# Performance work log

Measured on AMD Instinct MI355X. Metric: run time of the kernel, lower is better.

The kernel has to match this reference:

```python
import jax, jax.numpy as jnp
import numpy as np

TOP_K = 512  # int(node_num * K) = int(2048 * 0.25)
NEG = -1.0e12
SLOPE = 0.01  # nn.LeakyReLU default negative_slope


def setup_inputs() -> dict:
    key = jax.random.key(0)
    k1, k2, k3, k4 = jax.random.split(key, 4)
    B, N, in_c, out_c, gs = 8, 2048, 128, 128, 128
    x = jax.random.normal(k1, (B, N, in_c), dtype=jnp.float32)
    W = jax.random.normal(k2, (in_c, out_c), dtype=jnp.float32) * (1.0 / np.sqrt(in_c))
    a = jax.random.normal(k3, (2 * out_c, 1), dtype=jnp.float32) * (1.0 / np.sqrt(2 * out_c))
    GL = jax.random.normal(k4, (N, gs), dtype=jnp.float32) * (1.0 / np.sqrt(gs))
    return {"x": x, "W": W, "a": a, "GL": GL}


def reference(x, W, a, GL):
    B, N, _ = x.shape
    out_c = W.shape[1]
    # learned adjacency: softmax(relu(GL GL^T)) + I  -> [N, N]
    adj = jax.nn.softmax(jax.nn.relu(GL @ GL.T), axis=-1) + jnp.eye(N, dtype=GL.dtype)
    h = x @ W  # [B, N, out_c]
    # e[b,i,j] = LeakyReLU( [h_i ; h_j] . a ) = LeakyReLU( h_i.a1 + h_j.a2 )
    # (avoids materializing the [B, N*N, 2*out_c] concat of the original)
    a1, a2 = a[:out_c, 0], a[out_c:, 0]
    e = jax.nn.leaky_relu((h @ a1)[:, :, None] + (h @ a2)[:, None, :], SLOPE)  # [B,N,N]
    att = jnp.where(adj[None] > 0, e, NEG)
    # top-k along dim=1 (rows, per column j): transpose so that axis is last
    att_t = jnp.swapaxes(att, 1, 2)  # [B, Nj, Ni]
    _, idx = jax.lax.top_k(att_t, TOP_K)  # idx: [B, Nj, TOP_K]
    b_ix = jnp.arange(B)[:, None, None]
    j_ix = jnp.arange(N)[None, :, None]
    mask_t = jnp.zeros_like(att_t).at[b_ix, j_ix, idx].set(1.0)
    mask = jnp.swapaxes(mask_t, 1, 2)  # [B, Ni, Nj]
    att = jax.nn.softmax(att * mask, axis=2)
    h_prime = jax.nn.relu(att @ h)  # [B, N, out_c]
    return jnp.swapaxes(h_prime, -2, -1)  # [B, out_c, N]
```

## Files before the change

### kernel.cpp

```cpp
#include <hip/hip_runtime.h>
#include <math.h>


#define B_ 8
#define N_ 2048
#define C_ 128
#define TOPK_ 512
#define NCH_ 32
#define CL_ 64
#define NP1_ 2052
#define RANKB_ 256

#define H_OFF    ((size_t)0)
#define P_OFF    (H_OFF + (size_t)B_*N_*C_)
#define Q_OFF    (P_OFF + (size_t)B_*N_)
#define LOK_OFF  (Q_OFF + (size_t)B_*N_)
#define US_OFF   (LOK_OFF + (size_t)B_*N_)
#define VS_OFF   (US_OFF + (size_t)B_*N_)
#define SRT_OFF  (VS_OFF + (size_t)B_*N_)
#define SUS_OFF  (SRT_OFF + (size_t)B_*N_)
#define PVS_OFF  (SUS_OFF + (size_t)B_*NP1_)
#define SUL_OFF  (PVS_OFF + (size_t)B_*NP1_)
#define PVL_OFF  (SUL_OFF + (size_t)B_*N_*128)
#define TOTU_OFF (PVL_OFF + (size_t)B_*N_*128)
#define TOTV_OFF (TOTU_OFF + (size_t)B_*NCH_*128)
#define MPART_OFF (TOTV_OFF + (size_t)B_*NCH_*128)

__global__ __launch_bounds__(256) void k_pq(const float* __restrict__ x,
                                            const float* __restrict__ W,
                                            const float* __restrict__ a,
                                            float* __restrict__ p,
                                            float* __restrict__ q) {
  __shared__ float al[256];
  __shared__ float wa1[128], wa2[128];
  const int t = threadIdx.x;
  const int r0 = blockIdx.x * 64;
  al[t] = a[t];
  __syncthreads();
  if (t < 128) {
    const float* Wr = W + (size_t)t * 128;
    float s1 = 0.f, s2 = 0.f;
#pragma unroll
    for (int j = 0; j < 128; j += 4) {
      float4 wv = *(const float4*)(Wr + j);
      s1 = fmaf(wv.x, al[j + 0], s1);
      s1 = fmaf(wv.y, al[j + 1], s1);
      s1 = fmaf(wv.z, al[j + 2], s1);
      s1 = fmaf(wv.w, al[j + 3], s1);
      s2 = fmaf(wv.x, al[128 + j + 0], s2);
      s2 = fmaf(wv.y, al[128 + j + 1], s2);
      s2 = fmaf(wv.z, al[128 + j + 2], s2);
      s2 = fmaf(wv.w, al[128 + j + 3], s2);
    }
    wa1[t] = s1; wa2[t] = s2;
  }
  __syncthreads();
  const int row = t >> 2, part = t & 3;
  const float* xr = x + (size_t)(r0 + row) * 128 + part * 32;
  const float* w1 = wa1 + part * 32;
  const float* w2 = wa2 + part * 32;
  float sp = 0.f, sq = 0.f;
#pragma unroll
  for (int i = 0; i < 8; ++i) {
    float4 xv = *(const float4*)(xr + 4 * i);
    float4 w1v = *(const float4*)(w1 + 4 * i);
    float4 w2v = *(const float4*)(w2 + 4 * i);
    sp = fmaf(xv.x, w1v.x, sp); sp = fmaf(xv.y, w1v.y, sp);
    sp = fmaf(xv.z, w1v.z, sp); sp = fmaf(xv.w, w1v.w, sp);
    sq = fmaf(xv.x, w2v.x, sq); sq = fmaf(xv.y, w2v.y, sq);
    sq = fmaf(xv.z, w2v.z, sq); sq = fmaf(xv.w, w2v.w, sq);
  }
  sp += __shfl_xor(sp, 1, 64); sp += __shfl_xor(sp, 2, 64);
  sq += __shfl_xor(sq, 1, 64); sq += __shfl_xor(sq, 2, 64);
  if (part == 0) { p[r0 + row] = sp; q[r0 + row] = sq; }
}

__global__ __launch_bounds__(512, 4) void k_fuse(
    const float* __restrict__ x, const float* __restrict__ W,
    float* __restrict__ h, float* __restrict__ mpart,
    const float* __restrict__ q, const float* __restrict__ p,
    float* __restrict__ u_s, float* __restrict__ v_s,
    int* __restrict__ srt, int* __restrict__ lok) {
  union __align__(16) SMem {
    struct { float Wl[64 * 128]; float xl[64 * 68]; } g;
    struct { float ql[N_]; float pl[N_]; } r;
  };
  __shared__ SMem sm;
  const int blk = blockIdx.x, t = threadIdx.x;

  if (blk < RANKB_) {
    const int b = blk >> 5, tile = blk & 31;
    const int i0 = tile * 64;
    ((float4*)sm.r.ql)[t] = ((const float4*)(q + (size_t)b * N_))[t];
    ((float4*)sm.r.pl)[t] = ((const float4*)(p + (size_t)b * N_))[t];
    __syncthreads();
    const int row = t >> 3, s = t & 7;
    const int i = i0 + row;
    const float qi = sm.r.ql[i], pi = sm.r.pl[i];
    const float negpi = -pi;
    int qr = 0, lo = 0, pr = 0;
    for (int g = s; g < 512; g += 8) {
      float4 qj = ((const float4*)sm.r.ql)[g];
      float4 pj = ((const float4*)sm.r.pl)[g];
      const int j0 = 4 * g;
      qr += (qj.x < qi || (qj.x == qi && (j0 + 0) < i)) ? 1 : 0;
      qr += (qj.y < qi || (qj.y == qi && (j0 + 1) < i)) ? 1 : 0;
      qr += (qj.z < qi || (qj.z == qi && (j0 + 2) < i)) ? 1 : 0;
      qr += (qj.w < qi || (qj.w == qi && (j0 + 3) < i)) ? 1 : 0;
      lo += (qj.x < negpi) ? 1 : 0;
      lo += (qj.y < negpi) ? 1 : 0;
      lo += (qj.z < negpi) ? 1 : 0;
      lo += (qj.w < negpi) ? 1 : 0;
      pr += (pj.x > pi || (pj.x == pi && (j0 + 0) < i)) ? 1 : 0;
      pr += (pj.y > pi || (pj.y == pi && (j0 + 1) < i)) ? 1 : 0;
      pr += (pj.z > pi || (pj.z == pi && (j0 + 2) < i)) ? 1 : 0;
      pr += (pj.w > pi || (pj.w == pi && (j0 + 3) < i)) ? 1 : 0;
    }
    qr += __shfl_xor(qr, 1, 64); qr += __shfl_xor(qr, 2, 64); qr += __shfl_xor(qr, 4, 64);
    lo += __shfl_xor(lo, 1, 64); lo += __shfl_xor(lo, 2, 64); lo += __shfl_xor(lo, 4, 64);
    pr += __shfl_xor(pr, 1, 64); pr += __shfl_xor(pr, 2, 64); pr += __shfl_xor(pr, 4, 64);
    if (s == 0) {
      u_s[(size_t)b * N_ + qr] = __expf(qi);
      v_s[(size_t)b * N_ + qr] = __expf(0.01f * qi);
      srt[(size_t)b * N_ + qr] = i;
      lok[(size_t)b * N_ + i] = lo | ((pr < TOPK_) ? 0x10000 : 0);
    }
    return;
  }

  float* Wl = sm.g.Wl;
  float* xl = sm.g.xl;
  const int g = blk - RANKB_;
  const int r0 = g * 64;
  const int cg = t & 15, rp = (t >> 4) & 15;
  const bool act = t < 256;
  float acc[4][8];
#pragma unroll
  for (int r = 0; r < 4; ++r)
#pragma unroll
    for (int j = 0; j < 8; ++j) acc[r][j] = 0.f;

  for (int kc = 0; kc < 2; ++kc) {
    __syncthreads();
    const float4* W4 = (const float4*)(W + (size_t)kc * 64 * 128);
    float4* Wl4 = (float4*)Wl;
#pragma unroll
    for (int i = 0; i < 4; ++i) Wl4[t + 512 * i] = W4[t + 512 * i];
#pragma unroll
    for (int i = 0; i < 2; ++i) {
      int idx = t + 512 * i;
      int row = idx >> 4, c4i = idx & 15;
      float4 v = *(const float4*)(x + (size_t)(r0 + row) * 128 + kc * 64 + c4i * 4);
      ((float4*)xl)[row * 17 + c4i] = v;
    }
    __syncthreads();
    if (act) {
      for (int k = 0; k < 64; ++k) {
        const float4* Wr = (const float4*)(Wl + k * 128);
        float4 w0 = Wr[cg];
        float4 w1 = Wr[cg + 16];
#pragma unroll
        for (int r = 0; r < 4; ++r) {
          float xv = xl[(4 * rp + r) * 68 + k];
          acc[r][0] = fmaf(xv, w0.x, acc[r][0]);
          acc[r][1] = fmaf(xv, w0.y, acc[r][1]);
          acc[r][2] = fmaf(xv, w0.z, acc[r][2]);
          acc[r][3] = fmaf(xv, w0.w, acc[r][3]);
          acc[r][4] = fmaf(xv, w1.x, acc[r][4]);
          acc[r][5] = fmaf(xv, w1.y, acc[r][5]);
          acc[r][6] = fmaf(xv, w1.z, acc[r][6]);
          acc[r][7] = fmaf(xv, w1.w, acc[r][7]);
        }
      }
    }
  }
  const int c0 = 4 * cg, c1 = 4 * cg + 64;
  size_t hb = (size_t)r0 * 128;
  __syncthreads();
  float* scratch = xl;
  if (act) {
#pragma unroll
    for (int r = 0; r < 4; ++r) {
      int row = 4 * rp + r;
      *(float4*)(h + hb + (size_t)row * 128 + c0) =
          make_float4(acc[r][0], acc[r][1], acc[r][2], acc[r][3]);
      *(float4*)(h + hb + (size_t)row * 128 + c1) =
          make_float4(acc[r][4], acc[r][5], acc[r][6], acc[r][7]);
    }
#pragma unroll
    for (int j = 0; j < 4; ++j) {
      scratch[rp * 128 + c0 + j] = acc[0][j] + acc[1][j] + acc[2][j] + acc[3][j];
      scratch[rp * 128 + c1 + j] = acc[0][4 + j] + acc[1][4 + j] + acc[2][4 + j] + acc[3][4 + j];
    }
  }
  __syncthreads();
  if (t < 128) {
    float s = 0.f;
#pragma unroll
    for (int rr = 0; rr < 16; ++rr) s += scratch[rr * 128 + t];
    mpart[(size_t)g * 128 + t] = s;
  }
}

__global__ __launch_bounds__(256) void k_scan(const float* __restrict__ h,
                                              const float* __restrict__ u_s,
                                              const float* __restrict__ v_s,
                                              const int* __restrict__ srt,
                                              float* __restrict__ SUl,
                                              float* __restrict__ PVl,
                                              float* __restrict__ totU,
                                              float* __restrict__ totV,
                                              float* __restrict__ SUS,
                                              float* __restrict__ PVS) {
  __shared__ float hl[CL_][128];
  __shared__ float ul[CL_], vl[CL_];
  __shared__ int sl[CL_];
  __shared__ float2 sa[256], sb[256];
  const int t = threadIdx.x;
  if (blockIdx.x >= 256) {
    const int b = blockIdx.x - 256;
    float4 ua = ((const float4*)(u_s + (size_t)b * N_))[2 * t];
    float4 ub = ((const float4*)(u_s + (size_t)b * N_))[2 * t + 1];
    float4 wa = ((const float4*)(v_s + (size_t)b * N_))[2 * t];
    float4 wb = ((const float4*)(v_s + (size_t)b * N_))[2 * t + 1];
    float su = ua.x + ua.y + ua.z + ua.w + ub.x + ub.y + ub.z + ub.w;
    float sw = wa.x + wa.y + wa.z + wa.w + wb.x + wb.y + wb.z + wb.w;
    sa[t] = make_float2(su, sw);
    __syncthreads();
    float2* cur = sa; float2* nxt = sb;
    for (int off = 1; off < 256; off <<= 1) {
      float2 vv = cur[t];
      if (t >= off) { float2 o = cur[t - off]; vv.x += o.x; vv.y += o.y; }
      nxt[t] = vv;
      __syncthreads();
      float2* tmp = cur; cur = nxt; nxt = tmp;
    }
    float2 incl = cur[t];
    float2 tot = cur[255];
    float exclU = incl.x - su, exclW = incl.y - sw;
    float s0 = tot.x - exclU;
    float s1 = s0 - ua.x, s2 = s1 - ua.y, s3 = s2 - ua.z;
    float s4 = s3 - ua.w, s5 = s4 - ub.x, s6 = s5 - ub.y, s7 = s6 - ub.z;
    float p0 = exclW;
    float p1 = p0 + wa.x, p2 = p1 + wa.y, p3 = p2 + wa.z;
    float p4 = p3 + wa.w, p5 = p4 + wb.x, p6 = p5 + wb.y, p7 = p6 + wb.z;
    float* Sb = SUS + (size_t)b * NP1_ + 8 * t;
    float* Pb = PVS + (size_t)b * NP1_ + 8 * t;
    *(float4*)(Sb) = make_float4(s0, s1, s2, s3);
    *(float4*)(Sb + 4) = make_float4(s4, s5, s6, s7);
    *(float4*)(Pb) = make_float4(p0, p1, p2, p3);
    *(float4*)(Pb + 4) = make_float4(p4, p5, p6, p7);
    if (t == 255) {
      SUS[(size_t)b * NP1_ + N_] = 0.f;
      PVS[(size_t)b * NP1_ + N_] = tot.y;
    }
    return;
  }
  const int b = blockIdx.x >> 5, ch = blockIdx.x & 31;
  const int base = b * N_ + ch * CL_;
  if (t < CL_) { ul[t] = u_s[base + t]; vl[t] = v_s[base + t]; sl[t] = srt[base + t]; }
  __syncthreads();
  {
    const int c4 = t & 31, rr = t >> 5;
#pragma unroll
    for (int i = 0; i < 8; ++i) {
      int tt = rr + 8 * i;
      float4 v = *(const float4*)(h + ((size_t)b * N_ + sl[tt]) * 128 + 4 * c4);
      *(float4*)(&hl[tt][4 * c4]) = v;
    }
  }
  __syncthreads();
  if (t < 128) {
    const int c = t;
    float run = 0.f;
    for (int tt = CL_ - 1; tt >= 0; --tt) {
      run = fmaf(ul[tt], hl[tt][c], run);
      SUl[((size_t)(base + tt)) * 128 + c] = run;
    }
    totU[(size_t)(b * NCH_ + ch) * 128 + c] = run;
  } else {
    const int c = t - 128;
    float run2 = 0.f;
    for (int tt = 0; tt < CL_; ++tt) {
      PVl[((size_t)(base + tt)) * 128 + c] = run2;
      run2 = fmaf(vl[tt], hl[tt][c], run2);
    }
    totV[(size_t)(b * NCH_ + ch) * 128 + c] = run2;
  }
}

__global__ __launch_bounds__(256) void k_out(const float* __restrict__ p,
                                             const int* __restrict__ lok,
                                             const float* __restrict__ SUS,
                                             const float* __restrict__ PVS,
                                             const float* __restrict__ SUl,
                                             const float* __restrict__ PVl,
                                             const float* __restrict__ totU,
                                             const float* __restrict__ totV,
                                             const float* __restrict__ mpart,
                                             float* __restrict__ out) {
  __shared__ float res[64 * 129];
  __shared__ float CSUs[(NCH_ + 1) * 128];
  __shared__ float CPVs[(NCH_ + 1) * 128];
  __shared__ float mr[128];
  __shared__ float A_s[64], B_s[64], invD[64];
  __shared__ int lo_s[64], keep_s[64];
  const int b = blockIdx.x >> 5, tile = blockIdx.x & 31;
  const int t = threadIdx.x;
  const int i0 = tile * 64;
  if (t < 128) {
    float ms = 0.f;
#pragma unroll
    for (int j = 0; j < 32; ++j) ms += mpart[(size_t)(b * 32 + j) * 128 + t];
    mr[t] = fmaxf(ms * (1.0f / (float)N_), 0.f);
    float s = 0.f;
    CSUs[NCH_ * 128 + t] = 0.f;
    for (int cc = NCH_ - 1; cc >= 0; --cc) {
      s += totU[(size_t)(b * NCH_ + cc) * 128 + t];
      CSUs[cc * 128 + t] = s;
    }
  } else {
    const int c2 = t - 128;
    float s2 = 0.f;
    for (int cc = 0; cc < NCH_; ++cc) {
      CPVs[cc * 128 + c2] = s2;
      s2 += totV[(size_t)(b * NCH_ + cc) * 128 + c2];
    }
    CPVs[NCH_ * 128 + c2] = s2;
  }
  __syncthreads();
  if (t < 64) {
    float pv = p[b * N_ + i0 + t];
    int lk = lok[(size_t)b * N_ + i0 + t];
    keep_s[t] = (lk >> 16) & 1;
    int lo = lk & 0xFFFF;
    lo_s[t] = lo;
    float A = __expf(pv), Bv = __expf(0.01f * pv);
    A_s[t] = A; B_s[t] = Bv;
    float sus = SUS[(size_t)b * NP1_ + lo];
    float pvs = PVS[(size_t)b * NP1_ + lo];
    invD[t] = 1.0f / fmaf(A, sus, Bv * pvs);
  }
  __syncthreads();
  const int half = t >> 7, c = t & 127;
#pragma unroll 4
  for (int ii2 = 0; ii2 < 64; ii2 += 2) {
    int ii = ii2 + half;
    float outv;
    if (keep_s[ii]) {
      int lo = lo_s[ii];
      float A = A_s[ii], Bv = B_s[ii];
      float suc, pvc;
      if (lo < N_) {
        int chn = lo >> 6;
        size_t ro = ((size_t)(b * N_ + lo)) * 128;
        suc = SUl[ro + c] + CSUs[(chn + 1) * 128 + c];
        pvc = PVl[ro + c] + CPVs[chn * 128 + c];
      } else {
        suc = 0.f;
        pvc = CPVs[NCH_ * 128 + c];
      }
      outv = fmaxf(fmaf(A, suc, Bv * pvc) * invD[ii], 0.f);
    } else {
      outv = mr[c];
    }
    res[ii * 129 + c] = outv;
  }
  __syncthreads();
#pragma unroll
  for (int pass = 0; pass < 8; ++pass) {
    int cc = (t >> 4) + pass * 16;
    int ii4 = (t & 15) * 4;
    float4 v;
    v.x = res[(ii4 + 0) * 129 + cc];
    v.y = res[(ii4 + 1) * 129 + cc];
    v.z = res[(ii4 + 2) * 129 + cc];
    v.w = res[(ii4 + 3) * 129 + cc];
    *(float4*)(out + ((size_t)(b * C_ + cc)) * N_ + i0 + ii4) = v;
  }
}

extern "C" void kernel_launch(void* const* d_in, const int* in_sizes, int n_in,
                              void* d_out, int out_size, void* d_ws, size_t ws_size,
                              hipStream_t stream) {
  (void)in_sizes; (void)n_in; (void)out_size; (void)ws_size;
  const float* x = (const float*)d_in[0];
  const float* W = (const float*)d_in[1];
  const float* a = (const float*)d_in[2];
  float* out = (float*)d_out;
  float* ws = (float*)d_ws;

  float* h    = ws + H_OFF;
  float* p    = ws + P_OFF;
  float* q    = ws + Q_OFF;
  int*   lok  = (int*)(ws + LOK_OFF);
  float* u_s  = ws + US_OFF;
  float* v_s  = ws + VS_OFF;
  int*   srt  = (int*)(ws + SRT_OFF);
  float* SUS  = ws + SUS_OFF;
  float* PVS  = ws + PVS_OFF;
  float* SUl  = ws + SUL_OFF;
  float* PVl  = ws + PVL_OFF;
  float* totU = ws + TOTU_OFF;
  float* totV = ws + TOTV_OFF;
  float* mpart = ws + MPART_OFF;

  k_pq<<<dim3((B_ * N_) / 64), dim3(256), 0, stream>>>(x, W, a, p, q);
  k_fuse<<<dim3(RANKB_ + (B_ * N_) / 64), dim3(512), 0, stream>>>(
      x, W, h, mpart, q, p, u_s, v_s, srt, lok);
  k_scan<<<dim3(256 + B_), dim3(256), 0, stream>>>(h, u_s, v_s, srt, SUl, PVl, totU, totV, SUS, PVS);
  k_out<<<dim3(B_ * 32), dim3(256), 0, stream>>>(p, lok, SUS, PVS, SUl, PVl, totU, totV, mpart, out);
}
```

Baseline: 104.3 us.

## Merge four kernels into one cooperative persistent kernel with grid syncs

Replaces the four separate launches (pq, gemm+rank, scan, output) with a single cooperative kernel of 256 blocks × 512 threads. Grid-wide syncs separate the phases, and a per-phase launch path is kept as a fallback. The pq computation now runs inside the gemm blocks instead of as its own kernel. This removes launch overhead and the gaps between kernels, but the rank work that previously overlapped with the gemm blocks is now serialized behind a grid barrier, and 256-thread phases leave half of each block idle.

```diff
diff --git a/kernel.cpp b/kernel.cpp
--- a/kernel.cpp
+++ b/kernel.cpp
@@ -1,5 +1,8 @@
 #include <hip/hip_runtime.h>
+#include <hip/hip_cooperative_groups.h>
 #include <math.h>
+
+namespace cg = cooperative_groups;
 
 
 #define B_ 8
@@ -9,7 +12,7 @@
 #define NCH_ 32
 #define CL_ 64
 #define NP1_ 2052
-#define RANKB_ 256
+#define NBLK_ 256
 
 #define H_OFF    ((size_t)0)
 #define P_OFF    (H_OFF + (size_t)B_*N_*C_)
@@ -26,83 +29,157 @@
 #define TOTV_OFF (TOTU_OFF + (size_t)B_*NCH_*128)
 #define MPART_OFF (TOTV_OFF + (size_t)B_*NCH_*128)
 
-__global__ __launch_bounds__(256) void k_pq(const float* __restrict__ x,
-                                            const float* __restrict__ W,
-                                            const float* __restrict__ a,
-                                            float* __restrict__ p,
-                                            float* __restrict__ q) {
-  __shared__ float al[256];
-  __shared__ float wa1[128], wa2[128];
-  const int t = threadIdx.x;
-  const int r0 = blockIdx.x * 64;
-  al[t] = a[t];
-  __syncthreads();
-  if (t < 128) {
-    const float* Wr = W + (size_t)t * 128;
-    float s1 = 0.f, s2 = 0.f;
-#pragma unroll
-    for (int j = 0; j < 128; j += 4) {
-      float4 wv = *(const float4*)(Wr + j);
-      s1 = fmaf(wv.x, al[j + 0], s1);
-      s1 = fmaf(wv.y, al[j + 1], s1);
-      s1 = fmaf(wv.z, al[j + 2], s1);
-      s1 = fmaf(wv.w, al[j + 3], s1);
-      s2 = fmaf(wv.x, al[128 + j + 0], s2);
-      s2 = fmaf(wv.y, al[128 + j + 1], s2);
-      s2 = fmaf(wv.z, al[128 + j + 2], s2);
-      s2 = fmaf(wv.w, al[128 + j + 3], s2);
-    }
-    wa1[t] = s1; wa2[t] = s2;
+union SMem {
+  struct { float Wl[64 * 128]; float xl[64 * 68];
+           float al[256]; float wa1[128]; float wa2[128]; } g;
+  struct { float ql[N_]; float pl[N_]; } r;
+  struct { float hl[CL_][128]; float ul[CL_]; float vl[CL_]; int sl[CL_];
+           float2 sa[256]; float2 sb[256]; } s;
+  struct { float CSU[(NCH_ + 1) * 128]; float CPV[(NCH_ + 1) * 128];
+           float mr[128]; float A[64]; float Bv[64]; float invD[64];
+           int lo[64]; int keep[64]; float res[64 * 129]; } o;
+};
+
+__global__ __launch_bounds__(512, 4) void k_all(
+    const float* __restrict__ x, const float* __restrict__ W,
+    const float* __restrict__ a, float* __restrict__ out,
+    float* __restrict__ h, float* __restrict__ p, float* __restrict__ q,
+    int* __restrict__ lok, float* __restrict__ u_s, float* __restrict__ v_s,
+    int* __restrict__ srt, float* __restrict__ SUS, float* __restrict__ PVS,
+    float* __restrict__ SUl, float* __restrict__ PVl,
+    float* __restrict__ totU, float* __restrict__ totV,
+    float* __restrict__ mpart, int phase) {
+  __shared__ SMem sm;
+  cg::grid_group grid = cg::this_grid();
+  const int blk = blockIdx.x, t = threadIdx.x;
+  const bool all = (phase < 0);
+
+  if (all || phase == 0) {
+    const int r0 = blk * 64;
+    if (t < 256) sm.g.al[t] = a[t];
+    __syncthreads();
+    if (t < 128) {
+      const float* Wr = W + (size_t)t * 128;
+      float s1 = 0.f, s2 = 0.f;
+#pragma unroll
+      for (int j = 0; j < 128; j += 4) {
+        float4 wv = *(const float4*)(Wr + j);
+        s1 = fmaf(wv.x, sm.g.al[j + 0], s1);
+        s1 = fmaf(wv.y, sm.g.al[j + 1], s1);
+        s1 = fmaf(wv.z, sm.g.al[j + 2], s1);
+        s1 = fmaf(wv.w, sm.g.al[j + 3], s1);
+        s2 = fmaf(wv.x, sm.g.al[128 + j + 0], s2);
+        s2 = fmaf(wv.y, sm.g.al[128 + j + 1], s2);
+        s2 = fmaf(wv.z, sm.g.al[128 + j + 2], s2);
+        s2 = fmaf(wv.w, sm.g.al[128 + j + 3], s2);
+      }
+      sm.g.wa1[t] = s1; sm.g.wa2[t] = s2;
+    }
+    __syncthreads();
+    {
+      const int row = t >> 3, part = t & 7;
+      const float* xr = x + (size_t)(r0 + row) * 128 + part * 16;
+      const float* w1 = sm.g.wa1 + part * 16;
+      const float* w2 = sm.g.wa2 + part * 16;
+      float sp = 0.f, sq = 0.f;
+#pragma unroll
+      for (int i = 0; i < 4; ++i) {
+        float4 xv = *(const float4*)(xr + 4 * i);
+        float4 w1v = *(const float4*)(w1 + 4 * i);
+        float4 w2v = *(const float4*)(w2 + 4 * i);
+        sp = fmaf(xv.x, w1v.x, sp); sp = fmaf(xv.y, w1v.y, sp);
+        sp = fmaf(xv.z, w1v.z, sp); sp = fmaf(xv.w, w1v.w, sp);
+        sq = fmaf(xv.x, w2v.x, sq); sq = fmaf(xv.y, w2v.y, sq);
+        sq = fmaf(xv.z, w2v.z, sq); sq = fmaf(xv.w, w2v.w, sq);
+      }
+      sp += __shfl_xor(sp, 1, 64); sp += __shfl_xor(sp, 2, 64); sp += __shfl_xor(sp, 4, 64);
+      sq += __shfl_xor(sq, 1, 64); sq += __shfl_xor(sq, 2, 64); sq += __shfl_xor(sq, 4, 64);
+      if (part == 0) { p[r0 + row] = sp; q[r0 + row] = sq; }
+    }
+    const int cg2 = t & 15, rp = (t >> 4) & 15;
+    const bool act = t < 256;
+    float acc[4][8];
+#pragma unroll
+    for (int r = 0; r < 4; ++r)
+#pragma unroll
+      for (int j = 0; j < 8; ++j) acc[r][j] = 0.f;
+    for (int kc = 0; kc < 2; ++kc) {
+      __syncthreads();
+      const float4* W4 = (const float4*)(W + (size_t)kc * 64 * 128);
+      float4* Wl4 = (float4*)sm.g.Wl;
+#pragma unroll
+      for (int i = 0; i < 4; ++i) Wl4[t + 512 * i] = W4[t + 512 * i];
+#pragma unroll
+      for (int i = 0; i < 2; ++i) {
+        int idx = t + 512 * i;
+        int row = idx >> 4, c4i = idx & 15;
+        float4 v = *(const float4*)(x + (size_t)(r0 + row) * 128 + kc * 64 + c4i * 4);
+        ((float4*)sm.g.xl)[row * 17 + c4i] = v;
+      }
+      __syncthreads();
+      if (act) {
+        for (int k = 0; k < 64; ++k) {
+          const float4* Wr = (const float4*)(sm.g.Wl + k * 128);
+          float4 w0 = Wr[cg2];
+          float4 w1 = Wr[cg2 + 16];
+#pragma unroll
+          for (int r = 0; r < 4; ++r) {
+            float xv = sm.g.xl[(4 * rp + r) * 68 + k];
+            acc[r][0] = fmaf(xv, w0.x, acc[r][0]);
+            acc[r][1] = fmaf(xv, w0.y, acc[r][1]);
+            acc[r][2] = fmaf(xv, w0.z, acc[r][2]);
+            acc[r][3] = fmaf(xv, w0.w, acc[r][3]);
+            acc[r][4] = fmaf(xv, w1.x, acc[r][4]);
+            acc[r][5] = fmaf(xv, w1.y, acc[r][5]);
+            acc[r][6] = fmaf(xv, w1.z, acc[r][6]);
+            acc[r][7] = fmaf(xv, w1.w, acc[r][7]);
+          }
+        }
+      }
+    }
+    const int c0 = 4 * cg2, c1 = 4 * cg2 + 64;
+    size_t hb = (size_t)r0 * 128;
+    __syncthreads();
+    float* scratch = sm.g.xl;
+    if (act) {
+#pragma unroll
+      for (int r = 0; r < 4; ++r) {
+        int row = 4 * rp + r;
+        *(float4*)(h + hb + (size_t)row * 128 + c0) =
+            make_float4(acc[r][0], acc[r][1], acc[r][2], acc[r][3]);
+        *(float4*)(h + hb + (size_t)row * 128 + c1) =
+            make_float4(acc[r][4], acc[r][5], acc[r][6], acc[r][7]);
+      }
+#pragma unroll
+      for (int j = 0; j < 4; ++j) {
+        scratch[rp * 128 + c0 + j] = acc[0][j] + acc[1][j] + acc[2][j] + acc[3][j];
+        scratch[rp * 128 + c1 + j] = acc[0][4 + j] + acc[1][4 + j] + acc[2][4 + j] + acc[3][4 + j];
+      }
+    }
+    __syncthreads();
+    if (t < 128) {
+      float s = 0.f;
+#pragma unroll
+      for (int rr = 0; rr < 16; ++rr) s += scratch[rr * 128 + t];
+      mpart[(size_t)blk * 128 + t] = s;
+    }
   }
-  __syncthreads();
-  const int row = t >> 2, part = t & 3;
-  const float* xr = x + (size_t)(r0 + row) * 128 + part * 32;
-  const float* w1 = wa1 + part * 32;
-  const float* w2 = wa2 + part * 32;
-  float sp = 0.f, sq = 0.f;
-#pragma unroll
-  for (int i = 0; i < 8; ++i) {
-    float4 xv = *(const float4*)(xr + 4 * i);
-    float4 w1v = *(const float4*)(w1 + 4 * i);
-    float4 w2v = *(const float4*)(w2 + 4 * i);
-    sp = fmaf(xv.x, w1v.x, sp); sp = fmaf(xv.y, w1v.y, sp);
-    sp = fmaf(xv.z, w1v.z, sp); sp = fmaf(xv.w, w1v.w, sp);
-    sq = fmaf(xv.x, w2v.x, sq); sq = fmaf(xv.y, w2v.y, sq);
-    sq = fmaf(xv.z, w2v.z, sq); sq = fmaf(xv.w, w2v.w, sq);
-  }
-  sp += __shfl_xor(sp, 1, 64); sp += __shfl_xor(sp, 2, 64);
-  sq += __shfl_xor(sq, 1, 64); sq += __shfl_xor(sq, 2, 64);
-  if (part == 0) { p[r0 + row] = sp; q[r0 + row] = sq; }
-}
-
-__global__ __launch_bounds__(512, 4) void k_fuse(
-    const float* __restrict__ x, const float* __restrict__ W,
-    float* __restrict__ h, float* __restrict__ mpart,
-    const float* __restrict__ q, const float* __restrict__ p,
-    float* __restrict__ u_s, float* __restrict__ v_s,
-    int* __restrict__ srt, int* __restrict__ lok) {
-  union __align__(16) SMem {
-    struct { float Wl[64 * 128]; float xl[64 * 68]; } g;
-    struct { float ql[N_]; float pl[N_]; } r;
-  };
-  __shared__ SMem sm;
-  const int blk = blockIdx.x, t = threadIdx.x;
-
-  if (blk < RANKB_) {
-    const int b = blk >> 5, tile = blk & 31;
-    const int i0 = tile * 64;
+  if (all) grid.sync(); else if (phase == 0) return;
+
+  if (all || phase == 1) {
+    const int b = blk >> 5, i0 = (blk & 31) * 64;
     ((float4*)sm.r.ql)[t] = ((const float4*)(q + (size_t)b * N_))[t];
     ((float4*)sm.r.pl)[t] = ((const float4*)(p + (size_t)b * N_))[t];
     __syncthreads();
-    const int row = t >> 3, s = t & 7;
+    const int row = t >> 3, s8 = t & 7;
     const int i = i0 + row;
     const float qi = sm.r.ql[i], pi = sm.r.pl[i];
     const float negpi = -pi;
     int qr = 0, lo = 0, pr = 0;
-    for (int g = s; g < 512; g += 8) {
-      float4 qj = ((const float4*)sm.r.ql)[g];
-      float4 pj = ((const float4*)sm.r.pl)[g];
-      const int j0 = 4 * g;
+    for (int g2 = s8; g2 < 512; g2 += 8) {
+      float4 qj = ((const float4*)sm.r.ql)[g2];
+      float4 pj = ((const float4*)sm.r.pl)[g2];
+      const int j0 = 4 * g2;
       qr += (qj.x < qi || (qj.x == qi && (j0 + 0) < i)) ? 1 : 0;
       qr += (qj.y < qi || (qj.y == qi && (j0 + 1) < i)) ? 1 : 0;
       qr += (qj.z < qi || (qj.z == qi && (j0 + 2) < i)) ? 1 : 0;
@@ -119,264 +196,170 @@
     qr += __shfl_xor(qr, 1, 64); qr += __shfl_xor(qr, 2, 64); qr += __shfl_xor(qr, 4, 64);
     lo += __shfl_xor(lo, 1, 64); lo += __shfl_xor(lo, 2, 64); lo += __shfl_xor(lo, 4, 64);
     pr += __shfl_xor(pr, 1, 64); pr += __shfl_xor(pr, 2, 64); pr += __shfl_xor(pr, 4, 64);
-    if (s == 0) {
+    if (s8 == 0) {
       u_s[(size_t)b * N_ + qr] = __expf(qi);
       v_s[(size_t)b * N_ + qr] = __expf(0.01f * qi);
       srt[(size_t)b * N_ + qr] = i;
       lok[(size_t)b * N_ + i] = lo | ((pr < TOPK_) ? 0x10000 : 0);
     }
-    return;
   }
-
-  float* Wl = sm.g.Wl;
-  float* xl = sm.g.xl;
-  const int g = blk - RANKB_;
-  const int r0 = g * 64;
-  const int cg = t & 15, rp = (t >> 4) & 15;
-  const bool act = t < 256;
-  float acc[4][8];
-#pragma unroll
-  for (int r = 0; r < 4; ++r)
-#pragma unroll
-    for (int j = 0; j < 8; ++j) acc[r][j] = 0.f;
-
-  for (int kc = 0; kc < 2; ++kc) {
-    __syncthreads();
-    const float4* W4 = (const float4*)(W + (size_t)kc * 64 * 128);
-    float4* Wl4 = (float4*)Wl;
-#pragma unroll
-    for (int i = 0; i < 4; ++i) Wl4[t + 512 * i] = W4[t + 512 * i];
-#pragma unroll
-    for (int i = 0; i < 2; ++i) {
-      int idx = t + 512 * i;
-      int row = idx >> 4, c4i = idx & 15;
-      float4 v = *(const float4*)(x + (size_t)(r0 + row) * 128 + kc * 64 + c4i * 4);
-      ((float4*)xl)[row * 17 + c4i] = v;
-    }
-    __syncthreads();
-    if (act) {
-      for (int k = 0; k < 64; ++k) {
-        const float4* Wr = (const float4*)(Wl + k * 128);
-        float4 w0 = Wr[cg];
-        float4 w1 = Wr[cg + 16];
-#pragma unroll
-        for (int r = 0; r < 4; ++r) {
-          float xv = xl[(4 * rp + r) * 68 + k];
-          acc[r][0] = fmaf(xv, w0.x, acc[r][0]);
-          acc[r][1] = fmaf(xv, w0.y, acc[r][1]);
-          acc[r][2] = fmaf(xv, w0.z, acc[r][2]);
-          acc[r][3] = fmaf(xv, w0.w, acc[r][3]);
-          acc[r][4] = fmaf(xv, w1.x, acc[r][4]);
-          acc[r][5] = fmaf(xv, w1.y, acc[r][5]);
-          acc[r][6] = fmaf(xv, w1.z, acc[r][6]);
-          acc[r][7] = fmaf(xv, w1.w, acc[r][7]);
+  if (all) grid.sync(); else if (phase == 1) return;
+
+  if (all || phase == 2) {
+    const int b = blk >> 5, ch = blk & 31;
+    const int base = b * N_ + ch * CL_;
+    if (t < CL_) { sm.s.ul[t] = u_s[base + t]; sm.s.vl[t] = v_s[base + t]; sm.s.sl[t] = srt[base + t]; }
+    __syncthreads();
+    {
+      const int c4 = t & 31, rr = t >> 5;
+#pragma unroll
+      for (int i = 0; i < 4; ++i) {
+        int tt = rr + 16 * i;
+        float4 v = *(const float4*)(h + ((size_t)b * N_ + sm.s.sl[tt]) * 128 + 4 * c4);
+        *(float4*)(&sm.s.hl[tt][4 * c4]) = v;
+      }
+    }
+    __syncthreads();
+    if (blk < B_) {
+      const int b2 = blk;
+      float4 ua = {}, ub = {}, wa = {}, wb = {};
+      float su = 0.f, sw = 0.f;
+      if (t < 256) {
+        ua = ((const float4*)(u_s + (size_t)b2 * N_))[2 * t];
+        ub = ((const float4*)(u_s + (size_t)b2 * N_))[2 * t + 1];
+        wa = ((const float4*)(v_s + (size_t)b2 * N_))[2 * t];
+        wb = ((const float4*)(v_s + (size_t)b2 * N_))[2 * t + 1];
+        su = ua.x + ua.y + ua.z + ua.w + ub.x + ub.y + ub.z + ub.w;
+        sw = wa.x + wa.y + wa.z + wa.w + wb.x + wb.y + wb.z + wb.w;
+        sm.s.sa[t] = make_float2(su, sw);
+      }
+      __syncthreads();
+      float2* cur = sm.s.sa; float2* nxt = sm.s.sb;
+      for (int off = 1; off < 256; off <<= 1) {
+        if (t < 256) {
+          float2 vv = cur[t];
+          if (t >= off) { float2 o2 = cur[t - off]; vv.x += o2.x; vv.y += o2.y; }
+          nxt[t] = vv;
         }
-      }
+        __syncthreads();
+        float2* tmp = cur; cur = nxt; nxt = tmp;
+      }
+      if (t < 256) {
+        float2 incl = cur[t];
+        float2 tot = cur[255];
+        float exclU = incl.x - su, exclW = incl.y - sw;
+        float s0 = tot.x - exclU;
+        float s1 = s0 - ua.x, s2 = s1 - ua.y, s3 = s2 - ua.z;
+        float s4 = s3 - ua.w, s5 = s4 - ub.x, s6 = s5 - ub.y, s7 = s6 - ub.z;
+        float p0 = exclW;
+        float p1 = p0 + wa.x, p2 = p1 + wa.y, p3 = p2 + wa.z;
+        float p4 = p3 + wa.w, p5 = p4 + wb.x, p6 = p5 + wb.y, p7 = p6 + wb.z;
+        float* Sb = SUS + (size_t)b2 * NP1_ + 8 * t;
+        float* Pb = PVS + (size_t)b2 * NP1_ + 8 * t;
+        *(float4*)(Sb) = make_float4(s0, s1, s2, s3);
+        *(float4*)(Sb + 4) = make_float4(s4, s5, s6, s7);
+        *(float4*)(Pb) = make_float4(p0, p1, p2, p3);
+        *(float4*)(Pb + 4) = make_float4(p4, p5, p6, p7);
+        if (t == 255) {
+          SUS[(size_t)b2 * NP1_ + N_] = 0.f;
+          PVS[(size_t)b2 * NP1_ + N_] = tot.y;
+        }
+      }
+    }
+    if (t < 128) {
+      const int c = t;
+      float run = 0.f;
+      for (int tt = CL_ - 1; tt >= 0; --tt) {
+        run = fmaf(sm.s.ul[tt], sm.s.hl[tt][c], run);
+        SUl[((size_t)(base + tt)) * 128 + c] = run;
+      }
+      totU[(size_t)(b * NCH_ + ch) * 128 + c] = run;
+    } else if (t < 256) {
+      const int c = t - 128;
+      float run2 = 0.f;
+      for (int tt = 0; tt < CL_; ++tt) {
+        PVl[((size_t)(base + tt)) * 128 + c] = run2;
+        run2 = fmaf(sm.s.vl[tt], sm.s.hl[tt][c], run2);
+      }
+      totV[(size_t)(b * NCH_ + ch) * 128 + c] = run2;
     }
   }
-  const int c0 = 4 * cg, c1 = 4 * cg + 64;
-  size_t hb = (size_t)r0 * 128;
-  __syncthreads();
-  float* scratch = xl;
-  if (act) {
-#pragma unroll
-    for (int r = 0; r < 4; ++r) {
-      int row = 4 * rp + r;
-      *(float4*)(h + hb + (size_t)row * 128 + c0) =
-          make_float4(acc[r][0], acc[r][1], acc[r][2], acc[r][3]);
-      *(float4*)(h + hb + (size_t)row * 128 + c1) =
-          make_float4(acc[r][4], acc[r][5], acc[r][6], acc[r][7]);
-    }
-#pragma unroll
-    for (int j = 0; j < 4; ++j) {
-      scratch[rp * 128 + c0 + j] = acc[0][j] + acc[1][j] + acc[2][j] + acc[3][j];
-      scratch[rp * 128 + c1 + j] = acc[0][4 + j] + acc[1][4 + j] + acc[2][4 + j] + acc[3][4 + j];
-    }
-  }
-  __syncthreads();
-  if (t < 128) {
-    float s = 0.f;
-#pragma unroll
-    for (int rr = 0; rr < 16; ++rr) s += scratch[rr * 128 + t];
-    mpart[(size_t)g * 128 + t] = s;
-  }
-}
-
-__global__ __launch_bounds__(256) void k_scan(const float* __restrict__ h,
-                                              const float* __restrict__ u_s,
-                                              const float* __restrict__ v_s,
-                                              const int* __restrict__ srt,
-                                              float* __restrict__ SUl,
-                                              float* __restrict__ PVl,
-                                              float* __restrict__ totU,
-                                              float* __restrict__ totV,
-                                              float* __restrict__ SUS,
-                                              float* __restrict__ PVS) {
-  __shared__ float hl[CL_][128];
-  __shared__ float ul[CL_], vl[CL_];
-  __shared__ int sl[CL_];
-  __shared__ float2 sa[256], sb[256];
-  const int t = threadIdx.x;
-  if (blockIdx.x >= 256) {
-    const int b = blockIdx.x - 256;
-    float4 ua = ((const float4*)(u_s + (size_t)b * N_))[2 * t];
-    float4 ub = ((const float4*)(u_s + (size_t)b * N_))[2 * t + 1];
-    float4 wa = ((const float4*)(v_s + (size_t)b * N_))[2 * t];
-    float4 wb = ((const float4*)(v_s + (size_t)b * N_))[2 * t + 1];
-    float su = ua.x + ua.y + ua.z + ua.w + ub.x + ub.y + ub.z + ub.w;
-    float sw = wa.x + wa.y + wa.z + wa.w + wb.x + wb.y + wb.z + wb.w;
-    sa[t] = make_float2(su, sw);
-    __syncthreads();
-    float2* cur = sa; float2* nxt = sb;
-    for (int off = 1; off < 256; off <<= 1) {
-      float2 vv = cur[t];
-      if (t >= off) { float2 o = cur[t - off]; vv.x += o.x; vv.y += o.y; }
-      nxt[t] = vv;
-      __syncthreads();
-      float2* tmp = cur; cur = nxt; nxt = tmp;
-    }
-    float2 incl = cur[t];
-    float2 tot = cur[255];
-    float exclU = incl.x - su, exclW = incl.y - sw;
-    float s0 = tot.x - exclU;
-    float s1 = s0 - ua.x, s2 = s1 - ua.y, s3 = s2 - ua.z;
-    float s4 = s3 - ua.w, s5 = s4 - ub.x, s6 = s5 - ub.y, s7 = s6 - ub.z;
-    float p0 = exclW;
-    float p1 = p0 + wa.x, p2 = p1 + wa.y, p3 = p2 + wa.z;
-    float p4 = p3 + wa.w, p5 = p4 + wb.x, p6 = p5 + wb.y, p7 = p6 + wb.z;
-    float* Sb = SUS + (size_t)b * NP1_ + 8 * t;
-    float* Pb = PVS + (size_t)b * NP1_ + 8 * t;
-    *(float4*)(Sb) = make_float4(s0, s1, s2, s3);
-    *(float4*)(Sb + 4) = make_float4(s4, s5, s6, s7);
-    *(float4*)(Pb) = make_float4(p0, p1, p2, p3);
-    *(float4*)(Pb + 4) = make_float4(p4, p5, p6, p7);
-    if (t == 255) {
-      SUS[(size_t)b * NP1_ + N_] = 0.f;
-      PVS[(size_t)b * NP1_ + N_] = tot.y;
-    }
-    return;
-  }
-  const int b = blockIdx.x >> 5, ch = blockIdx.x & 31;
-  const int base = b * N_ + ch * CL_;
-  if (t < CL_) { ul[t] = u_s[base + t]; vl[t] = v_s[base + t]; sl[t] = srt[base + t]; }
-  __syncthreads();
-  {
-    const int c4 = t & 31, rr = t >> 5;
-#pragma unroll
-    for (int i = 0; i < 8; ++i) {
-      int tt = rr + 8 * i;
-      float4 v = *(const float4*)(h + ((size_t)b * N_ + sl[tt]) * 128 + 4 * c4);
-      *(float4*)(&hl[tt][4 * c4]) = v;
-    }
-  }
-  __syncthreads();
-  if (t < 128) {
-    const int c = t;
-    float run = 0.f;
-    for (int tt = CL_ - 1; tt >= 0; --tt) {
-      run = fmaf(ul[tt], hl[tt][c], run);
-      SUl[((size_t)(base + tt)) * 128 + c] = run;
-    }
-    totU[(size_t)(b * NCH_ + ch) * 128 + c] = run;
-  } else {
-    const int c = t - 128;
-    float run2 = 0.f;
-    for (int tt = 0; tt < CL_; ++tt) {
-      PVl[((size_t)(base + tt)) * 128 + c] = run2;
-      run2 = fmaf(vl[tt], hl[tt][c], run2);
-    }
-    totV[(size_t)(b * NCH_ + ch) * 128 + c] = run2;
-  }
-}
-
-__global__ __launch_bounds__(256) void k_out(const float* __restrict__ p,
-                                             const int* __restrict__ lok,
-                                             const float* __restrict__ SUS,
-                                             const float* __restrict__ PVS,
-                                             const float* __restrict__ SUl,
-                                             const float* __restrict__ PVl,
-                                             const float* __restrict__ totU,
-                                             const float* __restrict__ totV,
-                                             const float* __restrict__ mpart,
-                                             float* __restrict__ out) {
-  __shared__ float res[64 * 129];
-  __shared__ float CSUs[(NCH_ + 1) * 128];
-  __shared__ float CPVs[(NCH_ + 1) * 128];
-  __shared__ float mr[128];
-  __shared__ float A_s[64], B_s[64], invD[64];
-  __shared__ int lo_s[64], keep_s[64];
-  const int b = blockIdx.x >> 5, tile = blockIdx.x & 31;
-  const int t = threadIdx.x;
-  const int i0 = tile * 64;
-  if (t < 128) {
-    float ms = 0.f;
-#pragma unroll
-    for (int j = 0; j < 32; ++j) ms += mpart[(size_t)(b * 32 + j) * 128 + t];
-    mr[t] = fmaxf(ms * (1.0f / (float)N_), 0.f);
-    float s = 0.f;
-    CSUs[NCH_ * 128 + t] = 0.f;
-    for (int cc = NCH_ - 1; cc >= 0; --cc) {
-      s += totU[(size_t)(b * NCH_ + cc) * 128 + t];
-      CSUs[cc * 128 + t] = s;
-    }
-  } else {
-    const int c2 = t - 128;
-    float s2 = 0.f;
-    for (int cc = 0; cc < NCH_; ++cc) {
-      CPVs[cc * 128 + c2] = s2;
-      s2 += totV[(size_t)(b * NCH_ + cc) * 128 + c2];
-    }
-    CPVs[NCH_ * 128 + c2] = s2;
-  }
-  __syncthreads();
-  if (t < 64) {
-    float pv = p[b * N_ + i0 + t];
-    int lk = lok[(size_t)b * N_ + i0 + t];
-    keep_s[t] = (lk >> 16) & 1;
-    int lo = lk & 0xFFFF;
-    lo_s[t] = lo;
-    float A = __expf(pv), Bv = __expf(0.01f * pv);
-    A_s[t] = A; B_s[t] = Bv;
-    float sus = SUS[(size_t)b * NP1_ + lo];
-    float pvs = PVS[(size_t)b * NP1_ + lo];
-    invD[t] = 1.0f / fmaf(A, sus, Bv * pvs);
-  }
-  __syncthreads();
-  const int half = t >> 7, c = t & 127;
+  if (all) grid.sync(); else if (phase == 2) return;
+
+  if (all || phase == 3) {
+    const int b = blk >> 5, tile = blk & 31;
+    const int i0 = tile * 64;
+    if (t < 128) {
+      float ms = 0.f;
+#pragma unroll
+      for (int j = 0; j < 32; ++j) ms += mpart[(size_t)(b * 32 + j) * 128 + t];
+      sm.o.mr[t] = fmaxf(ms * (1.0f / (float)N_), 0.f);
+      float s = 0.f;
+      sm.o.CSU[NCH_ * 128 + t] = 0.f;
+      for (int cc = NCH_ - 1; cc >= 0; --cc) {
+        s += totU[(size_t)(b * NCH_ + cc) * 128 + t];
+        sm.o.CSU[cc * 128 + t] = s;
+      }
+    } else if (t < 256) {
+      const int c2 = t - 128;
+      float s2 = 0.f;
+      for (int cc = 0; cc < NCH_; ++cc) {
+        sm.o.CPV[cc * 128 + c2] = s2;
+        s2 += totV[(size_t)(b * NCH_ + cc) * 128 + c2];
+      }
+      sm.o.CPV[NCH_ * 128 + c2] = s2;
+    }
+    __syncthreads();
+    if (t < 64) {
+      float pv = p[b * N_ + i0 + t];
+      int lk = lok[(size_t)b * N_ + i0 + t];
+      sm.o.keep[t] = (lk >> 16) & 1;
+      int lo = lk & 0xFFFF;
+      sm.o.lo[t] = lo;
+      float A = __expf(pv), Bv = __expf(0.01f * pv);
+      sm.o.A[t] = A; sm.o.Bv[t] = Bv;
+      float sus = SUS[(size_t)b * NP1_ + lo];
+      float pvs = PVS[(size_t)b * NP1_ + lo];
+      sm.o.invD[t] = 1.0f / fmaf(A, sus, Bv * pvs);
+    }
+    __syncthreads();
+    const int quarter = t >> 7, c = t & 127;
 #pragma unroll 4
-  for (int ii2 = 0; ii2 < 64; ii2 += 2) {
-    int ii = ii2 + half;
-    float outv;
-    if (keep_s[ii]) {
-      int lo = lo_s[ii];
-      float A = A_s[ii], Bv = B_s[ii];
-      float suc, pvc;
-      if (lo < N_) {
-        int chn = lo >> 6;
-        size_t ro = ((size_t)(b * N_ + lo)) * 128;
-        suc = SUl[ro + c] + CSUs[(chn + 1) * 128 + c];
-        pvc = PVl[ro + c] + CPVs[chn * 128 + c];
+    for (int m = 0; m < 16; ++m) {
+      int ii = 4 * m + quarter;
+      float outv;
+      if (sm.o.keep[ii]) {
+        int lo = sm.o.lo[ii];
+        float A = sm.o.A[ii], Bv = sm.o.Bv[ii];
+        float suc, pvc;
+        if (lo < N_) {
+          int chn = lo >> 6;
+          size_t ro = ((size_t)(b * N_ + lo)) * 128;
+          suc = SUl[ro + c] + sm.o.CSU[(chn + 1) * 128 + c];
+          pvc = PVl[ro + c] + sm.o.CPV[chn * 128 + c];
+        } else {
+          suc = 0.f;
+          pvc = sm.o.CPV[NCH_ * 128 + c];
+        }
+        outv = fmaxf(fmaf(A, suc, Bv * pvc) * sm.o.invD[ii], 0.f);
       } else {
-        suc = 0.f;
-        pvc = CPVs[NCH_ * 128 + c];
-      }
-      outv = fmaxf(fmaf(A, suc, Bv * pvc) * invD[ii], 0.f);
-    } else {
-      outv = mr[c];
-    }
-    res[ii * 129 + c] = outv;
-  }
-  __syncthreads();
-#pragma unroll
-  for (int pass = 0; pass < 8; ++pass) {
-    int cc = (t >> 4) + pass * 16;
-    int ii4 = (t & 15) * 4;
-    float4 v;
-    v.x = res[(ii4 + 0) * 129 + cc];
-    v.y = res[(ii4 + 1) * 129 + cc];
-    v.z = res[(ii4 + 2) * 129 + cc];
-    v.w = res[(ii4 + 3) * 129 + cc];
-    *(float4*)(out + ((size_t)(b * C_ + cc)) * N_ + i0 + ii4) = v;
+        outv = sm.o.mr[c];
+      }
+      sm.o.res[ii * 129 + c] = outv;
+    }
+    __syncthreads();
+#pragma unroll
+    for (int pass = 0; pass < 4; ++pass) {
+      int idx = pass * 512 + t;
+      int cc = idx >> 4;
+      int ii4 = (idx & 15) * 4;
+      float4 v;
+      v.x = sm.o.res[(ii4 + 0) * 129 + cc];
+      v.y = sm.o.res[(ii4 + 1) * 129 + cc];
+      v.z = sm.o.res[(ii4 + 2) * 129 + cc];
+      v.w = sm.o.res[(ii4 + 3) * 129 + cc];
+      *(float4*)(out + ((size_t)(b * C_ + cc)) * N_ + i0 + ii4) = v;
+    }
   }
 }
 
@@ -405,9 +388,22 @@
   float* totV = ws + TOTV_OFF;
   float* mpart = ws + MPART_OFF;
 
-  k_pq<<<dim3((B_ * N_) / 64), dim3(256), 0, stream>>>(x, W, a, p, q);
-  k_fuse<<<dim3(RANKB_ + (B_ * N_) / 64), dim3(512), 0, stream>>>(
-      x, W, h, mpart, q, p, u_s, v_s, srt, lok);
-  k_scan<<<dim3(256 + B_), dim3(256), 0, stream>>>(h, u_s, v_s, srt, SUl, PVl, totU, totV, SUS, PVS);
-  k_out<<<dim3(B_ * 32), dim3(256), 0, stream>>>(p, lok, SUS, PVS, SUl, PVl, totU, totV, mpart, out);
+  int ph_all = -1;
+  void* args[] = {
+    (void*)&x, (void*)&W, (void*)&a, (void*)&out,
+    (void*)&h, (void*)&p, (void*)&q, (void*)&lok,
+    (void*)&u_s, (void*)&v_s, (void*)&srt, (void*)&SUS, (void*)&PVS,
+    (void*)&SUl, (void*)&PVl, (void*)&totU, (void*)&totV, (void*)&mpart,
+    (void*)&ph_all
+  };
+  hipError_t err = hipLaunchCooperativeKernel((const void*)k_all, dim3(NBLK_),
+                                              dim3(512), args, 0, stream);
+  if (err != hipSuccess) {
+    (void)hipGetLastError();
+    for (int ph = 0; ph < 4; ++ph) {
+      hipLaunchKernelGGL(k_all, dim3(NBLK_), dim3(512), 0, stream,
+                         x, W, a, out, h, p, q, lok, u_s, v_s, srt,
+                         SUS, PVS, SUl, PVl, totU, totV, mpart, ph);
+    }
+  }
 }
```

New measurement: 210.8 us. 102% more time.
